# Performance work log

Measured on AMD Instinct MI355X. Metric: run time of the kernel, lower is better.

## Reference

```python
import jax, jax.numpy as jnp
import numpy as np
from functools import partial

P, N, C, S = 16, 128, 256, 64
HID = C // 4  # squeeze=4
NEG_SLOPE = 0.01  # nn.LeakyReLU default


def conv1d(x, w, pad):
    # x: [n, c_in, s], w: [c_out, c_in, k]
    return jax.lax.conv_general_dilated(
        x, w, window_strides=(1,), padding=[(pad, pad)],
        dimension_numbers=('NCH', 'OIH', 'NCH'))


def leaky_relu(v):
    return jnp.where(v >= 0, v, NEG_SLOPE * v)


def pool_sum(x, k):
    # x: [p, n, c, s]; sum over window k along s with symmetric padding
    return jax.lax.reduce_window(
        x, 0.0, jax.lax.add, (1, 1, 1, k), (1, 1, 1, 1),
        [(0, 0), (0, 0), (0, 0), (k // 2, k // 2)])


def pool_max(x, k):
    return jax.lax.reduce_window(
        x, -jnp.inf, jax.lax.max, (1, 1, 1, k), (1, 1, 1, 1),
        [(0, 0), (0, 0), (0, 0), (k // 2, k // 2)])


def setup_inputs() -> dict:
    key = jax.random.key(0)
    ks = jax.random.split(key, 5)
    return {
        'x': jax.random.normal(ks[0], (P, N, C, S), dtype=jnp.float32),
        'w31_a': jax.random.normal(ks[1], (P, HID, C, 3), dtype=jnp.float32) * 0.05,
        'w31_b': jax.random.normal(ks[2], (P, C, HID, 1), dtype=jnp.float32) * 0.05,
        'w33_a': jax.random.normal(ks[3], (P, HID, C, 3), dtype=jnp.float32) * 0.05,
        'w33_b': jax.random.normal(ks[4], (P, C, HID, 3), dtype=jnp.float32) * 0.05,
    }


def reference(x, w31_a, w31_b, w33_a, w33_b):
    # x: [p, n, c, s]
    # Per-part gating convs, vmapped over the part dimension p.
    def branch(xp, wa, wb, pad_b):
        h = leaky_relu(conv1d(xp, wa, 1))
        return conv1d(h, wb, pad_b)

    logits3x1 = jax.vmap(partial(branch, pad_b=0))(x, w31_a, w31_b)  # [p,n,c,s]
    logits3x3 = jax.vmap(partial(branch, pad_b=1))(x, w33_a, w33_b)  # [p,n,c,s]

    # AvgPool1d (count_include_pad=True -> divide by k) + MaxPool1d
    feat3x1 = pool_sum(x, 3) / 3.0 + pool_max(x, 3)
    feat3x3 = pool_sum(x, 5) / 5.0 + pool_max(x, 5)

    gated = feat3x1 * jax.nn.sigmoid(logits3x1) + feat3x3 * jax.nn.sigmoid(logits3x3)
    return jnp.max(gated, axis=-1)  # [p, n, c]


if __name__ == '__main__':
    out = reference(**setup_inputs())
    print(out.shape)
```

## Files before the change

### kernel.cpp

```cpp
#include <hip/hip_runtime.h>

#define PP 16
#define NN 128
#define CC 256
#define SS 64
#define HH 64

typedef __attribute__((ext_vector_type(8))) short v8bf;
typedef __attribute__((ext_vector_type(16))) float f32x16;
typedef __attribute__((ext_vector_type(4))) unsigned short u16x4;

__device__ __forceinline__ unsigned short f2bf(float f) {
    unsigned u = __float_as_uint(f);
    return (unsigned short)((u + 0x7fffu + ((u >> 16) & 1u)) >> 16);
}

__device__ __forceinline__ unsigned cvtpk(float a, float b) {
    unsigned r;
    asm("v_cvt_pk_bf16_f32 %0, %1, %2" : "=v"(r) : "v"(a), "v"(b));
    return r;
}

__global__ void k_pack_all(const float* __restrict__ w31a, const float* __restrict__ w33a,
                           const float* __restrict__ w31b, const float* __restrict__ w33b,
                           unsigned short* __restrict__ wp1,
                           unsigned short* __restrict__ wp31,
                           unsigned short* __restrict__ wp33) {
    int b = blockIdx.x;
    int t = threadIdx.x;
    if (b < 256) {
        int u = b * 256 + t;
        int c_blk = u & 31;
        int hid   = (u >> 5) & 63;
        int p     = (u >> 11) & 15;
        int beta  = u >> 15;
        const float* src = (beta ? w33a : w31a) + ((size_t)(p * 64 + hid) * 256 + c_blk * 8) * 3;
        float f[24];
        #pragma unroll
        for (int i = 0; i < 6; ++i) *(float4*)(f + i * 4) = ((const float4*)src)[i];
        int ks   = c_blk >> 1;
        int lane = (hid & 31) + 32 * (c_blk & 1);
        int mi   = hid >> 5;
        v8bf* dst = (v8bf*)wp1;
        #pragma unroll
        for (int tp = 0; tp < 3; ++tp) {
            int4 r;
            r.x = cvtpk(f[0 * 3 + tp], f[1 * 3 + tp]);
            r.y = cvtpk(f[2 * 3 + tp], f[3 * 3 + tp]);
            r.z = cvtpk(f[4 * 3 + tp], f[5 * 3 + tp]);
            r.w = cvtpk(f[6 * 3 + tp], f[7 * 3 + tp]);
            *(int4*)&dst[(size_t)((((beta * 16 + p) * 3 + tp) * 16 + ks) * 2 + mi) * 64 + lane] = r;
        }
    } else if (b < 384) {
        int u = (b - 256) * 256 + t;
        int hid_blk = u & 7;
        int cout    = (u >> 3) & 255;
        int p       = u >> 11;
        const float* src = w31b + (size_t)(p * 256 + cout) * 64 + hid_blk * 8;
        float f[8];
        *(float4*)(f)     = ((const float4*)src)[0];
        *(float4*)(f + 4) = ((const float4*)src)[1];
        int ks   = hid_blk >> 1;
        int lane = (cout & 31) + 32 * (hid_blk & 1);
        int ct   = cout >> 5;
        int4 r;
        r.x = cvtpk(f[0], f[1]);
        r.y = cvtpk(f[2], f[3]);
        r.z = cvtpk(f[4], f[5]);
        r.w = cvtpk(f[6], f[7]);
        *(int4*)&((v8bf*)wp31)[(size_t)((p * 4 + ks) * 8 + ct) * 64 + lane] = r;
    } else {
        int u = (b - 384) * 256 + t;
        int hid_blk = u & 7;
        int cout    = (u >> 3) & 255;
        int p       = u >> 11;
        const float* src = w33b + ((size_t)(p * 256 + cout) * 64 + hid_blk * 8) * 3;
        float f[24];
        #pragma unroll
        for (int i = 0; i < 6; ++i) *(float4*)(f + i * 4) = ((const float4*)src)[i];
        int ks   = hid_blk >> 1;
        int lane = (cout & 31) + 32 * (hid_blk & 1);
        int ct   = cout >> 5;
        v8bf* dst = (v8bf*)wp33;
        #pragma unroll
        for (int tp = 0; tp < 3; ++tp) {
            int4 r;
            r.x = cvtpk(f[0 * 3 + tp], f[1 * 3 + tp]);
            r.y = cvtpk(f[2 * 3 + tp], f[3 * 3 + tp]);
            r.z = cvtpk(f[4 * 3 + tp], f[5 * 3 + tp]);
            r.w = cvtpk(f[6 * 3 + tp], f[7 * 3 + tp]);
            *(int4*)&dst[(size_t)(((p * 3 + tp) * 4 + ks) * 8 + ct) * 64 + lane] = r;
        }
    }
}

#define XB_ROWB 512
#define HB_OFF 34816
#define HB_ROWB 256
#define LDS_BYTES 51712

__global__ __launch_bounds__(512, 2)
void fused_mfma(const float* __restrict__ x,
                const unsigned short* __restrict__ wp1,
                const unsigned short* __restrict__ wp31,
                const unsigned short* __restrict__ wp33,
                float* __restrict__ out) {
    __shared__ __align__(16) char lds[LDS_BYTES];
    char* xb = lds;
    char* hb = lds + HB_OFF;
    float* tmp = (float*)(lds + HB_OFF);

    const int t = threadIdx.x;
    const int n = blockIdx.x, p = blockIdx.y;
    const int pn = p * NN + n;
    const int lane = t & 63;
    const int l31 = lane & 31, lhi5 = lane >> 5;
    const int w = t >> 6;
    const float4 z4 = make_float4(0.f, 0.f, 0.f, 0.f);

    if (t < 128) {
        int rr = t >> 5;
        int row = (rr < 2) ? rr : 64 + rr;
        *(float4*)(xb + row * XB_ROWB + (t & 31) * 16) = z4;
    }

    const float4* xsrc = (const float4*)x + (size_t)pn * 4096;
    for (int ch = 0; ch < 4; ++ch) {
        #pragma unroll
        for (int i = 0; i < 2; ++i) {
            int j = t + i * 512;
            *(float4*)((char*)tmp + j * 16) = xsrc[ch * 1024 + j];
        }
        __syncthreads();
        {
            int s = t & 63, cg = t >> 6;
            int row = s + 2;
            int col = (2 * (ch * 64 + cg * 8)) ^ ((row & 15) << 4);
            float f[8];
            #pragma unroll
            for (int k2 = 0; k2 < 8; ++k2) f[k2] = tmp[(cg * 8 + k2) * 64 + s];
            int4 vv;
            vv.x = cvtpk(f[0], f[1]);
            vv.y = cvtpk(f[2], f[3]);
            vv.z = cvtpk(f[4], f[5]);
            vv.w = cvtpk(f[6], f[7]);
            *(int4*)(xb + row * XB_ROWB + col) = vv;
        }
        __syncthreads();
    }

    if (t < 32) {
        int row = (t >> 4) ? 65 : 0;
        *(float4*)(hb + row * HB_ROWB + (t & 15) * 16) = z4;
    }

    {
        const int beta = w & 1, mi = (w >> 1) & 1, ni = (w >> 2) & 1;
        const v8bf* wv = (const v8bf*)wp1;
        const size_t abase = (size_t)((beta * 16 + p) * 3) * 32 * 64 + (size_t)mi * 64 + lane;
        f32x16 acc = {};
        #pragma unroll
        for (int tp = 0; tp < 3; ++tp) {
            int r = ni * 32 + l31 + tp + 1;
            int swz = (r & 15) << 4;
            const char* xrow = xb + r * XB_ROWB;
            #pragma unroll
            for (int ks = 0; ks < 16; ++ks) {
                v8bf A = wv[abase + (size_t)(tp * 16 + ks) * 128];
                v8bf B = *(const v8bf*)(xrow + ((2 * (ks * 16 + 8 * lhi5)) ^ swz));
                acc = __builtin_amdgcn_mfma_f32_32x32x16_bf16(A, B, acc, 0, 0, 0);
            }
        }
        int r2 = ni * 32 + l31 + 1;
        int swz2 = (r2 & 15) << 4;
        char* hrow = hb + r2 * HB_ROWB;
        #pragma unroll
        for (int rg = 0; rg < 4; ++rg) {
            int col = beta * 128 + 2 * (mi * 32 + 8 * rg + 4 * lhi5);
            float v[4];
            #pragma unroll
            for (int q = 0; q < 4; ++q) {
                float a = acc[rg * 4 + q];
                v[q] = a >= 0.f ? a : 0.01f * a;
            }
            int2 hv;
            hv.x = cvtpk(v[0], v[1]);
            hv.y = cvtpk(v[2], v[3]);
            *(int2*)(hrow + (col ^ swz2)) = hv;
        }
    }
    __syncthreads();

    {
        const int ct = w;
        const v8bf* w1v = (const v8bf*)wp31;
        const v8bf* w3v = (const v8bf*)wp33;
        float gm[16];
        #pragma unroll
        for (int i = 0; i < 16; ++i) gm[i] = -3.4e38f;

        #pragma unroll
        for (int ni = 0; ni < 2; ++ni) {
            const int s = ni * 32 + l31;
            f32x16 a31 = {};
            {
                int r = s + 1;
                int swz = (r & 15) << 4;
                const char* hrow = hb + r * HB_ROWB;
                #pragma unroll
                for (int ks = 0; ks < 4; ++ks) {
                    v8bf A = w1v[(size_t)((p * 4 + ks) * 8 + ct) * 64 + lane];
                    v8bf B = *(const v8bf*)(hrow + ((2 * (ks * 16 + 8 * lhi5)) ^ swz));
                    a31 = __builtin_amdgcn_mfma_f32_32x32x16_bf16(A, B, a31, 0, 0, 0);
                }
            }
            f32x16 a33 = {};
            #pragma unroll
            for (int tp = 0; tp < 3; ++tp) {
                int r = s + tp;
                int swz = (r & 15) << 4;
                const char* hrow = hb + r * HB_ROWB;
                #pragma unroll
                for (int ks = 0; ks < 4; ++ks) {
                    v8bf A = w3v[(size_t)(((p * 3 + tp) * 4 + ks) * 8 + ct) * 64 + lane];
                    v8bf B = *(const v8bf*)(hrow + ((128 + 2 * (ks * 16 + 8 * lhi5)) ^ swz));
                    a33 = __builtin_amdgcn_mfma_f32_32x32x16_bf16(A, B, a33, 0, 0, 0);
                }
            }
            #pragma unroll
            for (int rg = 0; rg < 4; ++rg) {
                int c0 = ct * 32 + 8 * rg + 4 * lhi5;
                float q[5][4];
                #pragma unroll
                for (int d = 0; d < 5; ++d) {
                    int r = s + d;
                    u16x4 hv = *(const u16x4*)(xb + r * XB_ROWB + ((2 * c0) ^ ((r & 15) << 4)));
                    #pragma unroll
                    for (int qi = 0; qi < 4; ++qi)
                        q[d][qi] = __uint_as_float((unsigned)hv[qi] << 16);
                }
                #pragma unroll
                for (int qi = 0; qi < 4; ++qi) {
                    int reg = rg * 4 + qi;
                    float xm2 = q[0][qi], xm = q[1][qi], x0 = q[2][qi], xp = q[3][qi], xp2 = q[4][qi];
                    float s3 = (xm + x0 + xp) * (1.f / 3.f);
                    float s5 = (xm2 + xm + x0 + xp + xp2) * 0.2f;
                    float m3 = x0;
                    if (s >= 1)  m3 = fmaxf(m3, xm);
                    if (s <= 62) m3 = fmaxf(m3, xp);
                    float m5 = m3;
                    if (s >= 2)  m5 = fmaxf(m5, xm2);
                    if (s <= 61) m5 = fmaxf(m5, xp2);
                    float s31 = __builtin_amdgcn_rcpf(1.f + __expf(-a31[reg]));
                    float s33 = __builtin_amdgcn_rcpf(1.f + __expf(-a33[reg]));
                    float g = (s3 + m3) * s31 + (s5 + m5) * s33;
                    gm[reg] = fmaxf(gm[reg], g);
                }
            }
        }
        #pragma unroll
        for (int reg = 0; reg < 16; ++reg) {
            float g = gm[reg];
            #pragma unroll
            for (int off = 16; off; off >>= 1) g = fmaxf(g, __shfl_xor(g, off));
            gm[reg] = g;
        }
        if (l31 == 0) {
            float* ob = out + (size_t)pn * 256 + ct * 32 + 4 * lhi5;
            #pragma unroll
            for (int rg = 0; rg < 4; ++rg) {
                float4 o = make_float4(gm[rg * 4], gm[rg * 4 + 1], gm[rg * 4 + 2], gm[rg * 4 + 3]);
                *(float4*)(ob + 8 * rg) = o;
            }
        }
    }
}

#define LW 72
__global__ __launch_bounds__(512, 2)
void fused_fallback(const float* __restrict__ x,
                    const float* __restrict__ w31a, const float* __restrict__ w31b,
                    const float* __restrict__ w33a, const float* __restrict__ w33b,
                    float* __restrict__ out) {
    __shared__ float lds[(CC + HH + HH) * LW];
    float* xs = lds;
    float* h31 = lds + CC * LW;
    float* h33 = h31 + HH * LW;
    const int t = threadIdx.x;
    const int n = blockIdx.x, p = blockIdx.y;
    const int lane = t & 63;
    {
        const float4* src = (const float4*)(x + (size_t)(p * NN + n) * (CC * SS));
        #pragma unroll
        for (int i = 0; i < 8; ++i) {
            int f4 = t + i * 512;
            int c = f4 >> 4, q = f4 & 15;
            *(float4*)(xs + c * LW + 4 + q * 4) = src[f4];
        }
        if (t < 256) {
            *(float4*)(xs + t * LW) = make_float4(0.f, 0.f, 0.f, 0.f);
            *(float4*)(xs + t * LW + 68) = make_float4(0.f, 0.f, 0.f, 0.f);
        } else if (t < 320) {
            int h = t - 256;
            *(float4*)(h33 + h * LW) = make_float4(0.f, 0.f, 0.f, 0.f);
            *(float4*)(h33 + h * LW + 68) = make_float4(0.f, 0.f, 0.f, 0.f);
        }
    }
    __syncthreads();
    {
        const int grp = t >> 6;
        const int conv = grp & 1;
        const int hid0 = (grp >> 1) * 16;
        const float4* wa4 = (const float4*)((conv ? w33a : w31a) + (size_t)p * (HH * CC * 3));
        float acc[16];
        #pragma unroll
        for (int h = 0; h < 16; ++h) acc[h] = 0.f;
        for (int c4 = 0; c4 < 64; ++c4) {
            float xm[4], x0[4], xp[4];
            #pragma unroll
            for (int j = 0; j < 4; ++j) {
                const float* r = xs + (c4 * 4 + j) * LW + 4 + lane;
                xm[j] = r[-1]; x0[j] = r[0]; xp[j] = r[1];
            }
            #pragma unroll
            for (int h = 0; h < 16; ++h) {
                const float4* wp = wa4 + (hid0 + h) * 192 + c4 * 3;
                float4 w0 = wp[0], w1 = wp[1], w2 = wp[2];
                float a = acc[h];
                a += xm[0]*w0.x + x0[0]*w0.y + xp[0]*w0.z;
                a += xm[1]*w0.w + x0[1]*w1.x + xp[1]*w1.y;
                a += xm[2]*w1.z + x0[2]*w1.w + xp[2]*w2.x;
                a += xm[3]*w2.y + x0[3]*w2.z + xp[3]*w2.w;
                acc[h] = a;
            }
        }
        float* dst = conv ? h33 : h31;
        #pragma unroll
        for (int h = 0; h < 16; ++h) {
            float v = acc[h];
            v = v >= 0.f ? v : 0.01f * v;
            dst[(hid0 + h) * LW + 4 + lane] = v;
        }
    }
    __syncthreads();
    {
        const int cg = t >> 6;
        const int c0 = cg * 32;
        float l31[32], l33[32];
        #pragma unroll
        for (int i = 0; i < 32; ++i) { l31[i] = 0.f; l33[i] = 0.f; }
        for (int hid = 0; hid < HH; ++hid) {
            const float* hr1 = h31 + hid * LW + 4 + lane;
            const float* hr3 = h33 + hid * LW + 4 + lane;
            float hv = hr1[0];
            float hm = hr3[-1], h0 = hr3[0], hp = hr3[1];
            #pragma unroll
            for (int i = 0; i < 32; ++i) {
                int c = c0 + i;
                l31[i] += hv * w31b[((size_t)p * 256 + c) * 64 + hid];
                const float* wb = w33b + (((size_t)p * 256 + c) * 64 + hid) * 3;
                l33[i] += hm * wb[0] + h0 * wb[1] + hp * wb[2];
            }
        }
        const size_t obase = ((size_t)p * NN + n) * CC + c0;
        #pragma unroll
        for (int i = 0; i < 32; ++i) {
            const float* r = xs + (c0 + i) * LW + 4 + lane;
            float xm2 = r[-2], xm = r[-1], x0v = r[0], xp = r[1], xp2 = r[2];
            float s3 = (xm + x0v + xp) * (1.f / 3.f);
            float s5 = (xm2 + xm + x0v + xp + xp2) * 0.2f;
            float m3 = x0v;
            if (lane >= 1)  m3 = fmaxf(m3, xm);
            if (lane <= 62) m3 = fmaxf(m3, xp);
            float m5 = m3;
            if (lane >= 2)  m5 = fmaxf(m5, xm2);
            if (lane <= 61) m5 = fmaxf(m5, xp2);
            float g = (s3 + m3) / (1.f + __expf(-l31[i])) + (s5 + m5) / (1.f + __expf(-l33[i]));
            #pragma unroll
            for (int off = 32; off; off >>= 1)
                g = fmaxf(g, __shfl_xor(g, off));
            if (lane == 0) out[obase + i] = g;
        }
    }
}

extern "C" void kernel_launch(void* const* d_in, const int* in_sizes, int n_in,
                              void* d_out, int out_size, void* d_ws, size_t ws_size,
                              hipStream_t stream) {
    const float* x    = (const float*)d_in[0];
    const float* w31a = (const float*)d_in[1];
    const float* w31b = (const float*)d_in[2];
    const float* w33a = (const float*)d_in[3];
    const float* w33b = (const float*)d_in[4];
    float* out = (float*)d_out;

    const size_t need = 5242880;
    dim3 grid(NN, PP);
    if (ws_size >= need) {
        unsigned short* wp1  = (unsigned short*)d_ws;
        unsigned short* wp31 = (unsigned short*)((char*)d_ws + 3145728);
        unsigned short* wp33 = (unsigned short*)((char*)d_ws + 3670016);
        k_pack_all<<<512, 256, 0, stream>>>(w31a, w33a, w31b, w33b, wp1, wp31, wp33);
        fused_mfma<<<grid, 512, 0, stream>>>(x, wp1, wp31, wp33, out);
    } else {
        fused_fallback<<<grid, 512, 0, stream>>>(x, w31a, w31b, w33a, w33b, out);
    }
}
```

Before: 260.1 us.

## Load x tiles via global_load_lds and share B operand across two MFMA accumulators

The x staging copy now uses the global_load_lds builtin to write global data straight into LDS, skipping the register round-trip. The first-layer conv now runs on 4 waves instead of 8. Each wave reuses one B fragment from LDS for two MFMAs, one per branch (31 and 33), with two accumulators, which halves B reads from LDS but leaves half the block idle in that phase. The pooling max/sum code is rewritten branch-free with select operations and reuses the 3-tap sum.

```diff
diff --git a/kernel.cpp b/kernel.cpp
--- a/kernel.cpp
+++ b/kernel.cpp
@@ -9,11 +9,6 @@
 typedef __attribute__((ext_vector_type(8))) short v8bf;
 typedef __attribute__((ext_vector_type(16))) float f32x16;
 typedef __attribute__((ext_vector_type(4))) unsigned short u16x4;
-
-__device__ __forceinline__ unsigned short f2bf(float f) {
-    unsigned u = __float_as_uint(f);
-    return (unsigned short)((u + 0x7fffu + ((u >> 16) & 1u)) >> 16);
-}
 
 __device__ __forceinline__ unsigned cvtpk(float a, float b) {
     unsigned r;
@@ -128,8 +123,11 @@
     for (int ch = 0; ch < 4; ++ch) {
         #pragma unroll
         for (int i = 0; i < 2; ++i) {
-            int j = t + i * 512;
-            *(float4*)((char*)tmp + j * 16) = xsrc[ch * 1024 + j];
+            const float4* gp = xsrc + ch * 1024 + i * 512 + t;
+            char* lp = (char*)tmp + i * 8192 + w * 1024;
+            __builtin_amdgcn_global_load_lds(
+                (const __attribute__((address_space(1))) void*)gp,
+                (__attribute__((address_space(3))) void*)lp, 16, 0, 0);
         }
         __syncthreads();
         {
@@ -154,11 +152,12 @@
         *(float4*)(hb + row * HB_ROWB + (t & 15) * 16) = z4;
     }
 
-    {
-        const int beta = w & 1, mi = (w >> 1) & 1, ni = (w >> 2) & 1;
+    if (w < 4) {
+        const int mi = w & 1, ni = (w >> 1) & 1;
         const v8bf* wv = (const v8bf*)wp1;
-        const size_t abase = (size_t)((beta * 16 + p) * 3) * 32 * 64 + (size_t)mi * 64 + lane;
-        f32x16 acc = {};
+        const size_t ab0 = (size_t)((0 * 16 + p) * 3) * 2048 + (size_t)mi * 64 + lane;
+        const size_t ab1 = (size_t)((1 * 16 + p) * 3) * 2048 + (size_t)mi * 64 + lane;
+        f32x16 acc0 = {}, acc1 = {};
         #pragma unroll
         for (int tp = 0; tp < 3; ++tp) {
             int r = ni * 32 + l31 + tp + 1;
@@ -166,9 +165,11 @@
             const char* xrow = xb + r * XB_ROWB;
             #pragma unroll
             for (int ks = 0; ks < 16; ++ks) {
-                v8bf A = wv[abase + (size_t)(tp * 16 + ks) * 128];
                 v8bf B = *(const v8bf*)(xrow + ((2 * (ks * 16 + 8 * lhi5)) ^ swz));
-                acc = __builtin_amdgcn_mfma_f32_32x32x16_bf16(A, B, acc, 0, 0, 0);
+                v8bf A0 = wv[ab0 + (size_t)(tp * 16 + ks) * 128];
+                acc0 = __builtin_amdgcn_mfma_f32_32x32x16_bf16(A0, B, acc0, 0, 0, 0);
+                v8bf A1 = wv[ab1 + (size_t)(tp * 16 + ks) * 128];
+                acc1 = __builtin_amdgcn_mfma_f32_32x32x16_bf16(A1, B, acc1, 0, 0, 0);
             }
         }
         int r2 = ni * 32 + l31 + 1;
@@ -176,17 +177,19 @@
         char* hrow = hb + r2 * HB_ROWB;
         #pragma unroll
         for (int rg = 0; rg < 4; ++rg) {
-            int col = beta * 128 + 2 * (mi * 32 + 8 * rg + 4 * lhi5);
-            float v[4];
+            int colbase = 2 * (mi * 32 + 8 * rg + 4 * lhi5);
+            float v0[4], v1[4];
             #pragma unroll
             for (int q = 0; q < 4; ++q) {
-                float a = acc[rg * 4 + q];
-                v[q] = a >= 0.f ? a : 0.01f * a;
-            }
-            int2 hv;
-            hv.x = cvtpk(v[0], v[1]);
-            hv.y = cvtpk(v[2], v[3]);
-            *(int2*)(hrow + (col ^ swz2)) = hv;
+                float a0 = acc0[rg * 4 + q], a1 = acc1[rg * 4 + q];
+                v0[q] = a0 >= 0.f ? a0 : 0.01f * a0;
+                v1[q] = a1 >= 0.f ? a1 : 0.01f * a1;
+            }
+            int2 h0, h1;
+            h0.x = cvtpk(v0[0], v0[1]); h0.y = cvtpk(v0[2], v0[3]);
+            h1.x = cvtpk(v1[0], v1[1]); h1.y = cvtpk(v1[2], v1[3]);
+            *(int2*)(hrow + (colbase ^ swz2)) = h0;
+            *(int2*)(hrow + ((128 + colbase) ^ swz2)) = h1;
         }
     }
     __syncthreads();
@@ -243,14 +246,15 @@
                 for (int qi = 0; qi < 4; ++qi) {
                     int reg = rg * 4 + qi;
                     float xm2 = q[0][qi], xm = q[1][qi], x0 = q[2][qi], xp = q[3][qi], xp2 = q[4][qi];
-                    float s3 = (xm + x0 + xp) * (1.f / 3.f);
-                    float s5 = (xm2 + xm + x0 + xp + xp2) * 0.2f;
-                    float m3 = x0;
-                    if (s >= 1)  m3 = fmaxf(m3, xm);
-                    if (s <= 62) m3 = fmaxf(m3, xp);
-                    float m5 = m3;
-                    if (s >= 2)  m5 = fmaxf(m5, xm2);
-                    if (s <= 61) m5 = fmaxf(m5, xp2);
+                    float sum3 = xm + x0 + xp;
+                    float s3 = sum3 * (1.f / 3.f);
+                    float s5 = (sum3 + xm2 + xp2) * 0.2f;
+                    float a_ = (s >= 1)  ? xm  : x0;
+                    float b_ = (s <= 62) ? xp  : x0;
+                    float m3 = fmaxf(fmaxf(a_, x0), b_);
+                    float c_ = (s >= 2)  ? xm2 : x0;
+                    float d_ = (s <= 61) ? xp2 : x0;
+                    float m5 = fmaxf(fmaxf(m3, c_), d_);
                     float s31 = __builtin_amdgcn_rcpf(1.f + __expf(-a31[reg]));
                     float s33 = __builtin_amdgcn_rcpf(1.f + __expf(-a33[reg]));
                     float g = (s3 + m3) * s31 + (s5 + m5) * s33;
```

Measured after the change: 268.0 us. 1.03x slower.
